# Kernel tuning notes

Hardware: AMD Instinct MI355X
Metric: run time of the kernel (lower is better)

Reference implementation:

```python
import jax, jax.numpy as jnp
import numpy as np

N = 50000   # nodes
E = 600000  # edges (avg degree 12)
D = 128     # feature dim (input_dim == output_dim for residual)
G = 8       # graphs in batch
EPS = 1e-5


def setup_inputs() -> dict:
    key = jax.random.key(0)
    ks = jax.random.split(key, 8)
    x = jax.random.normal(ks[0], (N, D), dtype=jnp.float32)
    edge_index = jax.random.randint(ks[1], (2, E), 0, N)
    batch = jnp.sort(jax.random.randint(ks[2], (N,), 0, G))
    s = 1.0 / np.sqrt(D)
    Wl = jax.random.normal(ks[3], (D, D), dtype=jnp.float32) * s
    bl = jax.random.normal(ks[4], (D,), dtype=jnp.float32) * s
    Wr = jax.random.normal(ks[5], (D, D), dtype=jnp.float32) * s
    return {
        "x": x,
        "edge_index": edge_index,
        "batch": batch,
        "num_graphs": G,
        "Wl": Wl,
        "bl": bl,
        "Wr": Wr,
        "gn_weight": jnp.ones((D,), jnp.float32),
        "gn_bias": jnp.zeros((D,), jnp.float32),
        "mean_scale": jnp.ones((D,), jnp.float32),
    }


def reference(x, edge_index, batch, num_graphs, Wl, bl, Wr, gn_weight, gn_bias, mean_scale):
    n = x.shape[0]
    src, dst = edge_index[0], edge_index[1]

    # SAGEConv: mean-aggregate neighbor (source) features at target nodes
    ones_e = jnp.ones(src.shape[0], dtype=x.dtype)
    deg = jax.ops.segment_sum(ones_e, dst, num_segments=n)          # [N]
    agg = jax.ops.segment_sum(x[src], dst, num_segments=n)          # [N, D]
    agg = agg / jnp.maximum(deg, 1.0)[:, None]
    f = agg @ Wl.T + bl + x @ Wr.T                                  # lin_l(agg) + lin_r(x)

    # exact (erf) GELU, as torch F.gelu default
    f = jax.nn.gelu(f, approximate=False)

    # GraphNorm: per-graph statistics with learnable mean_scale
    ones_n = jnp.ones(n, dtype=x.dtype)
    cnt = jax.ops.segment_sum(ones_n, batch, num_segments=num_graphs)[:, None]  # [G,1]
    mean = jax.ops.segment_sum(f, batch, num_segments=num_graphs) / cnt         # [G,D]
    out = f - mean_scale * mean[batch]
    var = jax.ops.segment_sum(out * out, batch, num_segments=num_graphs) / cnt  # [G,D]
    out = out / jnp.sqrt(var[batch] + EPS) * gn_weight + gn_bias

    # dropout is identity in eval mode; residual add
    return out + x
```

## Files before the change

kernel.cpp:

```cpp
#include <hip/hip_runtime.h>

#define D 128
#define NGRAPH 8
#define EPS 1e-5f
#define CAP 48

typedef __attribute__((ext_vector_type(4))) float f32x4;
typedef __attribute__((ext_vector_type(2))) float f32x2;
typedef __attribute__((ext_vector_type(8))) short s16x8;

__device__ __forceinline__ unsigned short f2bf(float f) {
    unsigned int u = __float_as_uint(f);
    u += 0x7fffu + ((u >> 16) & 1u);
    return (unsigned short)(u >> 16);
}

__global__ __launch_bounds__(256) void prep_fill_kernel(
    const float* __restrict__ Wl, const float* __restrict__ Wr,
    unsigned short* __restrict__ Bsw,
    const float* __restrict__ x, unsigned int* __restrict__ xb,
    unsigned int* __restrict__ xf8,
    const int* __restrict__ batch, int* __restrict__ bnd,
    const int* __restrict__ ei, int* __restrict__ cnt, int* __restrict__ adj,
    int N, int E, int Npad, int fillB)
{
    int b = blockIdx.x;
    if (b < 128) {
        int t = b * 256 + threadIdx.x;
        int j    = t & 7;
        int ln   = (t >> 3) & 63;
        int ks   = (t >> 9) & 7;
        int tile = t >> 12;
        int k = ks * 32 + (ln >> 4) * 8 + j;
        int d = tile * 16 + (ln & 15);
        float v = (k < 128) ? Wl[(size_t)d * 128 + k] : Wr[(size_t)d * 128 + (k - 128)];
        Bsw[t] = f2bf(v);
    } else if (b == 128) {
        int g = threadIdx.x;
        if (g <= NGRAPH) {
            int lo = 0, hi = N;
            while (lo < hi) {
                int mid = (lo + hi) >> 1;
                if (batch[mid] < g) lo = mid + 1; else hi = mid;
            }
            bnd[g] = lo;
        }
    } else if (b < 129 + fillB) {
        int e = (b - 129) * 256 + threadIdx.x;
        if (e < E) {
            int dst = ei[E + e];
            int pos = atomicAdd(&cnt[dst], 1);
            if (pos < CAP) adj[(size_t)dst * CAP + pos] = ei[e];
        }
    } else {
        int iu = (b - 129 - fillB) * 256 + threadIdx.x;
        if (iu < Npad * 32) {
            int n = iu >> 5, slot = iu & 31;
            if (iu < N * 32) {
                float4 p = *(const float4*)(x + (size_t)iu * 4);
                uint2 o;
                o.x = (unsigned int)f2bf(p.x) | ((unsigned int)f2bf(p.y) << 16);
                o.y = (unsigned int)f2bf(p.z) | ((unsigned int)f2bf(p.w) << 16);
                *(uint2*)(xb + (size_t)iu * 2) = o;
                int u8 = __builtin_amdgcn_cvt_pk_fp8_f32(p.x, p.y, 0, false);
                u8     = __builtin_amdgcn_cvt_pk_fp8_f32(p.z, p.w, u8, true);
                xf8[(size_t)n * 32 + slot] = (unsigned int)u8;
            } else {
                *(uint2*)(xb + (size_t)iu * 2) = make_uint2(0u, 0u);
                xf8[(size_t)n * 32 + slot] = 0u;
            }
        }
    }
}

__global__ __launch_bounds__(256) void aggregate_kernel(
    const unsigned short* __restrict__ xf8, const int* __restrict__ cnt,
    const int* __restrict__ adj, unsigned int* __restrict__ Aag, int N, int Npad)
{
    int n = blockIdx.x * 4 + (threadIdx.x >> 6);
    int lane = threadIdx.x & 63;
    if (n >= Npad) return;
    if (n >= N) { Aag[(size_t)n * 64 + lane] = 0u; return; }
    int deg = cnt[n];
    int lim = deg < CAP ? deg : CAP;
    int v = (lane < lim) ? adj[(size_t)n * CAP + lane] : 0;
    float a0 = 0.0f, a1 = 0.0f;
    int i = 0;
    for (; i + 8 <= lim; i += 8) {
        int nb[8];
#pragma unroll
        for (int k = 0; k < 8; ++k) nb[k] = __shfl(v, i + k, 64);
        unsigned short u[8];
#pragma unroll
        for (int k = 0; k < 8; ++k) u[k] = xf8[(size_t)nb[k] * 64 + lane];
#pragma unroll
        for (int k = 0; k < 8; ++k) {
            f32x2 d2 = __builtin_amdgcn_cvt_pk_f32_fp8((int)(unsigned int)u[k], false);
            a0 += d2[0]; a1 += d2[1];
        }
    }
    for (; i < lim; ++i) {
        int nb = __shfl(v, i, 64);
        f32x2 d2 = __builtin_amdgcn_cvt_pk_f32_fp8(
            (int)(unsigned int)xf8[(size_t)nb * 64 + lane], false);
        a0 += d2[0]; a1 += d2[1];
    }
    float inv = 1.0f / (float)(deg > 0 ? deg : 1);
    Aag[(size_t)n * 64 + lane] =
        (unsigned int)f2bf(a0 * inv) | ((unsigned int)f2bf(a1 * inv) << 16);
}

__global__ __launch_bounds__(256, 8) void gemm_kernel(
    const unsigned short* __restrict__ Aag, const unsigned short* __restrict__ xb16,
    const unsigned short* __restrict__ Bsw, const float* __restrict__ bl,
    const int* __restrict__ batch,
    float* __restrict__ gsum, float* __restrict__ gsumsq,
    float* __restrict__ fout, int N)
{
    int wave = threadIdx.x >> 6, lane = threadIdx.x & 63;
    int row0 = blockIdx.x * 32 + (wave >> 1) * 16;
    int th = wave & 1;
    int m = lane & 15, quad = lane >> 4;
    int r = row0 + m;

    s16x8 afrag[8];
    const unsigned short* ab = Aag + (size_t)r * 128 + quad * 8;
#pragma unroll
    for (int ks = 0; ks < 4; ++ks) afrag[ks] = *(const s16x8*)(ab + ks * 32);
    const unsigned short* xp = xb16 + (size_t)r * 128 + quad * 8;
#pragma unroll
    for (int ks = 0; ks < 4; ++ks) afrag[4 + ks] = *(const s16x8*)(xp + ks * 32);

    int nbase = row0;
    bool uni = (nbase + 15 < N) && (batch[nbase] == batch[nbase + 15]);
    int gu = (nbase < N) ? batch[nbase] : 0;

#pragma unroll
    for (int t = 0; t < 4; ++t) {
        int tile = th * 4 + t;
        f32x4 acc = {0.0f, 0.0f, 0.0f, 0.0f};
        const s16x8* bptr = (const s16x8*)Bsw + (size_t)(tile * 8) * 64 + lane;
#pragma unroll
        for (int ks = 0; ks < 8; ++ks)
            acc = __builtin_amdgcn_mfma_f32_16x16x32_bf16(afrag[ks], bptr[(size_t)ks * 64], acc, 0, 0, 0);
        int d = tile * 16 + m;
        float bias = bl[d];
        float sm = 0.0f, sq = 0.0f;
#pragma unroll
        for (int rr = 0; rr < 4; ++rr) {
            int node = nbase + quad * 4 + rr;
            float v = acc[rr] + bias;
            float g = 0.5f * v * (1.0f + erff(v * 0.70710678118654752f));
            if (node < N) {
                fout[(size_t)node * D + d] = g;
                if (uni) { sm += g; sq += g * g; }
                else {
                    int gg = batch[node];
                    unsafeAtomicAdd(&gsum[gg * D + d], g);
                    unsafeAtomicAdd(&gsumsq[gg * D + d], g * g);
                }
            }
        }
        if (uni) {
            sm += __shfl_xor(sm, 16, 64); sm += __shfl_xor(sm, 32, 64);
            sq += __shfl_xor(sq, 16, 64); sq += __shfl_xor(sq, 32, 64);
            if (quad == 0) {
                unsafeAtomicAdd(&gsum[gu * D + d], sm);
                unsafeAtomicAdd(&gsumsq[gu * D + d], sq);
            }
        }
    }
}

__global__ __launch_bounds__(256) void final_kernel(
    const float* __restrict__ f, const float* __restrict__ x,
    const int* __restrict__ batch, const int* __restrict__ bnd,
    const float* __restrict__ gsum, const float* __restrict__ gsumsq,
    const float* __restrict__ ms,
    const float* __restrict__ gw, const float* __restrict__ gb,
    float* __restrict__ out, int N)
{
    int t = blockIdx.x * 256 + threadIdx.x;
    if (t >= N * (D / 4)) return;
    int n  = t >> 5;
    int d0 = (t & 31) * 4;
    int g  = batch[n];
    int c  = bnd[g + 1] - bnd[g];
    float invc = 1.0f / (float)(c > 0 ? c : 1);
    size_t row = (size_t)n * D + d0;
    float4 fv = *(const float4*)(f + row);
    float4 xv = *(const float4*)(x + row);
    float4 s1 = *(const float4*)(gsum + g * D + d0);
    float4 s2 = *(const float4*)(gsumsq + g * D + d0);
    float4 msv = *(const float4*)(ms + d0);
    float4 gwv = *(const float4*)(gw + d0);
    float4 gbv = *(const float4*)(gb + d0);
    float4 o;
    {
        float mu = s1.x * invc, q = s2.x * invc, a = msv.x * mu;
        float sc = rsqrtf(q - 2.0f * a * mu + a * a + EPS);
        o.x = (fv.x - a) * sc * gwv.x + gbv.x + xv.x;
    }
    {
        float mu = s1.y * invc, q = s2.y * invc, a = msv.y * mu;
        float sc = rsqrtf(q - 2.0f * a * mu + a * a + EPS);
        o.y = (fv.y - a) * sc * gwv.y + gbv.y + xv.y;
    }
    {
        float mu = s1.z * invc, q = s2.z * invc, a = msv.z * mu;
        float sc = rsqrtf(q - 2.0f * a * mu + a * a + EPS);
        o.z = (fv.z - a) * sc * gwv.z + gbv.z + xv.z;
    }
    {
        float mu = s1.w * invc, q = s2.w * invc, a = msv.w * mu;
        float sc = rsqrtf(q - 2.0f * a * mu + a * a + EPS);
        o.w = (fv.w - a) * sc * gwv.w + gbv.w + xv.w;
    }
    *(float4*)(out + row) = o;
}

extern "C" void kernel_launch(void* const* d_in, const int* in_sizes, int n_in,
                              void* d_out, int out_size, void* d_ws, size_t ws_size,
                              hipStream_t stream)
{
    const float* x     = (const float*)d_in[0];
    const int*   ei    = (const int*)d_in[1];
    const int*   batch = (const int*)d_in[2];
    const float* Wl = (const float*)d_in[4];
    const float* bl = (const float*)d_in[5];
    const float* Wr = (const float*)d_in[6];
    const float* gw = (const float*)d_in[7];
    const float* gb = (const float*)d_in[8];
    const float* ms = (const float*)d_in[9];
    float* out = (float*)d_out;

    int N = in_sizes[0] / D;
    int E = in_sizes[1] / 2;
    int NBLK = (N + 63) / 64;
    int Npad = NBLK * 64;
    int NB32 = Npad / 32;

    float*          fout = (float*)d_ws;
    unsigned int*   xf8  = (unsigned int*)fout;
    unsigned int*   xb   = (unsigned int*)(fout + (size_t)Npad * D);
    unsigned short* Bsw  = (unsigned short*)(xb + (size_t)Npad * 64);
    float* gsum   = (float*)(Bsw + 32768);
    float* gsumsq = gsum + NGRAPH * D;
    unsigned int* pad = (unsigned int*)(gsumsq + NGRAPH * D);
    int*   cnt    = (int*)(pad + 4);
    int*   bnd    = cnt + N;
    int*   adj    = bnd + (NGRAPH + 1);
    unsigned int* Aag = (unsigned int*)(adj + (size_t)N * CAP);

    hipMemsetAsync(gsum, 0,
                   (2 * NGRAPH * D) * sizeof(float) + 4 * sizeof(unsigned int)
                   + (size_t)N * sizeof(int), stream);

    int fillB = (E + 255) / 256;
    int xbB   = (Npad * 32 + 255) / 256;
    prep_fill_kernel<<<129 + fillB + xbB, 256, 0, stream>>>(
        Wl, Wr, Bsw, x, xb, xf8, batch, bnd, ei, cnt, adj, N, E, Npad, fillB);

    aggregate_kernel<<<Npad / 4, 256, 0, stream>>>(
        (const unsigned short*)xf8, cnt, adj, Aag, N, Npad);

    gemm_kernel<<<NB32, 256, 0, stream>>>(
        (const unsigned short*)Aag, (const unsigned short*)xb, Bsw, bl,
        batch, gsum, gsumsq, fout, N);

    {
        int threads = N * (D / 4);
        final_kernel<<<(threads + 255) / 256, 256, 0, stream>>>(
            fout, x, batch, bnd, gsum, gsumsq, ms, gw, gb, out, N);
    }
}
```

Before: 193.5 us.

## Fuse neighbor aggregation into GEMM via LDS and store GELU output as bf16

The aggregation and GEMM kernels are merged. Each 256-thread block first gathers and mean-reduces 32 nodes' neighbor features into shared memory, then feeds the MFMA GEMM directly from LDS. This removes the global Aag round-trip and one launch. The GELU output is also stored as bf16 instead of fp32, halving the intermediate write and read in the final kernel, at the cost of extra rounding error in the normalized output. Grouping aggregation per 32-node block reduces gather parallelism per block and may lower latency hiding.

```diff
diff --git a/kernel.cpp b/kernel.cpp
--- a/kernel.cpp
+++ b/kernel.cpp
@@ -14,6 +14,8 @@
     u += 0x7fffu + ((u >> 16) & 1u);
     return (unsigned short)(u >> 16);
 }
+__device__ __forceinline__ float blo(unsigned int u) { return __uint_as_float(u << 16); }
+__device__ __forceinline__ float bhi(unsigned int u) { return __uint_as_float(u & 0xffff0000u); }
 
 __global__ __launch_bounds__(256) void prep_fill_kernel(
     const float* __restrict__ Wl, const float* __restrict__ Wr,
@@ -73,60 +75,63 @@
     }
 }
 
-__global__ __launch_bounds__(256) void aggregate_kernel(
+__global__ __launch_bounds__(256, 8) void fused_kernel(
     const unsigned short* __restrict__ xf8, const int* __restrict__ cnt,
-    const int* __restrict__ adj, unsigned int* __restrict__ Aag, int N, int Npad)
-{
-    int n = blockIdx.x * 4 + (threadIdx.x >> 6);
-    int lane = threadIdx.x & 63;
-    if (n >= Npad) return;
-    if (n >= N) { Aag[(size_t)n * 64 + lane] = 0u; return; }
-    int deg = cnt[n];
-    int lim = deg < CAP ? deg : CAP;
-    int v = (lane < lim) ? adj[(size_t)n * CAP + lane] : 0;
-    float a0 = 0.0f, a1 = 0.0f;
-    int i = 0;
-    for (; i + 8 <= lim; i += 8) {
-        int nb[8];
-#pragma unroll
-        for (int k = 0; k < 8; ++k) nb[k] = __shfl(v, i + k, 64);
-        unsigned short u[8];
-#pragma unroll
-        for (int k = 0; k < 8; ++k) u[k] = xf8[(size_t)nb[k] * 64 + lane];
-#pragma unroll
-        for (int k = 0; k < 8; ++k) {
-            f32x2 d2 = __builtin_amdgcn_cvt_pk_f32_fp8((int)(unsigned int)u[k], false);
+    const int* __restrict__ adj,
+    const unsigned short* __restrict__ xb16, const unsigned short* __restrict__ Bsw,
+    const float* __restrict__ bl, const int* __restrict__ batch,
+    float* __restrict__ gsum, float* __restrict__ gsumsq,
+    unsigned short* __restrict__ fout16, int N)
+{
+    __shared__ unsigned int aggL[32][68];
+
+    int wave = threadIdx.x >> 6, lane = threadIdx.x & 63;
+    int nblk0 = blockIdx.x * 32;
+
+#pragma unroll
+    for (int s = 0; s < 8; ++s) {
+        int ln = wave * 8 + s;
+        int node = nblk0 + ln;
+        int dg = (node < N) ? cnt[node] : 0;
+        int lm = dg < CAP ? dg : CAP;
+        int v = (lane < lm) ? adj[(size_t)node * CAP + lane] : 0;
+        float a0 = 0.0f, a1 = 0.0f;
+        int i = 0;
+        for (; i + 8 <= lm; i += 8) {
+            int nb[8];
+#pragma unroll
+            for (int k = 0; k < 8; ++k) nb[k] = __shfl(v, i + k, 64);
+            unsigned short u[8];
+#pragma unroll
+            for (int k = 0; k < 8; ++k) u[k] = xf8[(size_t)nb[k] * 64 + lane];
+#pragma unroll
+            for (int k = 0; k < 8; ++k) {
+                f32x2 d2 = __builtin_amdgcn_cvt_pk_f32_fp8((int)(unsigned int)u[k], false);
+                a0 += d2[0]; a1 += d2[1];
+            }
+        }
+        for (; i < lm; ++i) {
+            int nb = __shfl(v, i, 64);
+            f32x2 d2 = __builtin_amdgcn_cvt_pk_f32_fp8(
+                (int)(unsigned int)xf8[(size_t)nb * 64 + lane], false);
             a0 += d2[0]; a1 += d2[1];
         }
-    }
-    for (; i < lim; ++i) {
-        int nb = __shfl(v, i, 64);
-        f32x2 d2 = __builtin_amdgcn_cvt_pk_f32_fp8(
-            (int)(unsigned int)xf8[(size_t)nb * 64 + lane], false);
-        a0 += d2[0]; a1 += d2[1];
-    }
-    float inv = 1.0f / (float)(deg > 0 ? deg : 1);
-    Aag[(size_t)n * 64 + lane] =
-        (unsigned int)f2bf(a0 * inv) | ((unsigned int)f2bf(a1 * inv) << 16);
-}
-
-__global__ __launch_bounds__(256, 8) void gemm_kernel(
-    const unsigned short* __restrict__ Aag, const unsigned short* __restrict__ xb16,
-    const unsigned short* __restrict__ Bsw, const float* __restrict__ bl,
-    const int* __restrict__ batch,
-    float* __restrict__ gsum, float* __restrict__ gsumsq,
-    float* __restrict__ fout, int N)
-{
-    int wave = threadIdx.x >> 6, lane = threadIdx.x & 63;
-    int row0 = blockIdx.x * 32 + (wave >> 1) * 16;
+        float iv = 1.0f / (float)(dg > 0 ? dg : 1);
+        aggL[ln][lane] =
+            (unsigned int)f2bf(a0 * iv) | ((unsigned int)f2bf(a1 * iv) << 16);
+    }
+    __syncthreads();
+
+    int row0 = nblk0 + (wave >> 1) * 16;
     int th = wave & 1;
     int m = lane & 15, quad = lane >> 4;
     int r = row0 + m;
+    int lr = (wave >> 1) * 16 + m;
 
     s16x8 afrag[8];
-    const unsigned short* ab = Aag + (size_t)r * 128 + quad * 8;
-#pragma unroll
-    for (int ks = 0; ks < 4; ++ks) afrag[ks] = *(const s16x8*)(ab + ks * 32);
+#pragma unroll
+    for (int ks = 0; ks < 4; ++ks)
+        afrag[ks] = *(const s16x8*)&aggL[lr][ks * 16 + quad * 4];
     const unsigned short* xp = xb16 + (size_t)r * 128 + quad * 8;
 #pragma unroll
     for (int ks = 0; ks < 4; ++ks) afrag[4 + ks] = *(const s16x8*)(xp + ks * 32);
@@ -152,7 +157,7 @@
             float v = acc[rr] + bias;
             float g = 0.5f * v * (1.0f + erff(v * 0.70710678118654752f));
             if (node < N) {
-                fout[(size_t)node * D + d] = g;
+                fout16[(size_t)node * 128 + d] = f2bf(g);
                 if (uni) { sm += g; sq += g * g; }
                 else {
                     int gg = batch[node];
@@ -173,7 +178,7 @@
 }
 
 __global__ __launch_bounds__(256) void final_kernel(
-    const float* __restrict__ f, const float* __restrict__ x,
+    const unsigned int* __restrict__ f16, const float* __restrict__ x,
     const int* __restrict__ batch, const int* __restrict__ bnd,
     const float* __restrict__ gsum, const float* __restrict__ gsumsq,
     const float* __restrict__ ms,
@@ -188,7 +193,8 @@
     int c  = bnd[g + 1] - bnd[g];
     float invc = 1.0f / (float)(c > 0 ? c : 1);
     size_t row = (size_t)n * D + d0;
-    float4 fv = *(const float4*)(f + row);
+    uint2 fu = *(const uint2*)(f16 + (size_t)n * 64 + (d0 >> 1));
+    float4 fv = make_float4(blo(fu.x), bhi(fu.x), blo(fu.y), bhi(fu.y));
     float4 xv = *(const float4*)(x + row);
     float4 s1 = *(const float4*)(gsum + g * D + d0);
     float4 s2 = *(const float4*)(gsumsq + g * D + d0);
@@ -240,9 +246,9 @@
     int Npad = NBLK * 64;
     int NB32 = Npad / 32;
 
-    float*          fout = (float*)d_ws;
-    unsigned int*   xf8  = (unsigned int*)fout;
-    unsigned int*   xb   = (unsigned int*)(fout + (size_t)Npad * D);
+    unsigned int*   fout16 = (unsigned int*)d_ws;
+    unsigned int*   xf8  = fout16 + (size_t)Npad * 64;
+    unsigned int*   xb   = xf8 + (size_t)Npad * 32;
     unsigned short* Bsw  = (unsigned short*)(xb + (size_t)Npad * 64);
     float* gsum   = (float*)(Bsw + 32768);
     float* gsumsq = gsum + NGRAPH * D;
@@ -250,7 +256,6 @@
     int*   cnt    = (int*)(pad + 4);
     int*   bnd    = cnt + N;
     int*   adj    = bnd + (NGRAPH + 1);
-    unsigned int* Aag = (unsigned int*)(adj + (size_t)N * CAP);
 
     hipMemsetAsync(gsum, 0,
                    (2 * NGRAPH * D) * sizeof(float) + 4 * sizeof(unsigned int)
@@ -261,16 +266,14 @@
     prep_fill_kernel<<<129 + fillB + xbB, 256, 0, stream>>>(
         Wl, Wr, Bsw, x, xb, xf8, batch, bnd, ei, cnt, adj, N, E, Npad, fillB);
 
-    aggregate_kernel<<<Npad / 4, 256, 0, stream>>>(
-        (const unsigned short*)xf8, cnt, adj, Aag, N, Npad);
-
-    gemm_kernel<<<NB32, 256, 0, stream>>>(
-        (const unsigned short*)Aag, (const unsigned short*)xb, Bsw, bl,
-        batch, gsum, gsumsq, fout, N);
+    fused_kernel<<<NB32, 256, 0, stream>>>(
+        (const unsigned short*)xf8, cnt, adj,
+        (const unsigned short*)xb, Bsw, bl, batch,
+        gsum, gsumsq, (unsigned short*)fout16, N);
 
     {
         int threads = N * (D / 4);
         final_kernel<<<(threads + 255) / 256, 256, 0, stream>>>(
-            fout, x, batch, bnd, gsum, gsumsq, ms, gw, gb, out, N);
-    }
-}
+            fout16, x, batch, bnd, gsum, gsumsq, ms, gw, gb, out, N);
+    }
+}
```

Result: faster. 184.0 us (-4.9%).
